# Performance work log

Hardware: AMD Instinct MI355X
Metric: run time of the kernel (lower is better)

Reference implementation:

```python
import jax, jax.numpy as jnp
from jax import lax
import numpy as np

C = 64      # channels
K = 3       # dynamic kernel size
N = 2       # batch
H = 256
W = 256
DOWN = 4    # avgpool factor


def _conv(x, w, b):
    # 'SAME' padding matches get_same_padding for odd kernels, dilation=1
    y = lax.conv_general_dilated(x, w, (1, 1), 'SAME',
                                 dimension_numbers=('NCHW', 'OIHW', 'NCHW'))
    return y + b[None, :, None, None]


def _resblock(x, w1, b1, w2, b2):
    out = jax.nn.leaky_relu(_conv(x, w1, b1), 0.1)
    return _conv(out, w2, b2) + x


def _block(x, ws1, bs1, ws2, bs2):
    # fixed small loop over 3 structurally distinct ResBlocks
    for i in range(ws1.shape[0]):
        x = _resblock(x, ws1[i], bs1[i], ws2[i], bs2[i])
    return x


def _avgpool(x, k):
    n, c, h, w = x.shape
    return x.reshape(n, c, h // k, k, w // k, k).mean(axis=(3, 5))


def _maxpool(x, k):
    n, c, h, w = x.shape
    return x.reshape(n, c, h // k, k, w // k, k).max(axis=(3, 5))


def _dyn_conv(x, wt, k):
    # per-pixel depthwise conv: out[n,c,h,w] = sum_{dh,dw} xpad[n,c,h+dh,w+dw] * wt[n, c*k*k + dh*k + dw, h, w]
    # (torch's unfold/permute flattening pairs feat tap (dh,dw) with kernel channel index dh*k+dw)
    n, c, h, w = x.shape
    pad = (k - 1) // 2
    xp = jnp.pad(x, ((0, 0), (0, 0), (pad, pad), (pad, pad)), mode='edge')  # replicate pad
    wr = wt.reshape(n, c, k * k, h, w)
    out = jnp.zeros_like(x)
    for dh in range(k):            # fixed 3x3 tap loop; avoids materializing the unfold tensor
        for dw in range(k):
            out = out + xp[:, :, dh:dh + h, dw:dw + w] * wr[:, :, dh * k + dw]
    return out


def setup_inputs() -> dict:
    key = jax.random.key(0)
    ks = jax.random.split(key, 11)
    s = 0.05  # small init so 6 residual blocks stay numerically tame
    return {
        'x': jax.random.normal(ks[0], (N, C, H, W), jnp.float32),
        'blk1_w1': jax.random.normal(ks[1], (3, C, C, K, K), jnp.float32) * s,
        'blk1_b1': jnp.zeros((3, C), jnp.float32),
        'blk1_w2': jax.random.normal(ks[2], (3, C, C, K, K), jnp.float32) * s,
        'blk1_b2': jnp.zeros((3, C), jnp.float32),
        'blk2_w1': jax.random.normal(ks[3], (3, C, C, K, K), jnp.float32) * s,
        'blk2_b1': jnp.zeros((3, C), jnp.float32),
        'blk2_w2': jax.random.normal(ks[4], (3, C, C, K, K), jnp.float32) * s,
        'blk2_b2': jnp.zeros((3, C), jnp.float32),
        'tok_w': jax.random.normal(ks[5], (K * K * C, C, 1, 1), jnp.float32) * s,
        'tok_b': jnp.zeros((K * K * C,), jnp.float32),
    }


def reference(x, blk1_w1, blk1_b1, blk1_w2, blk1_b2,
              blk2_w1, blk2_b1, blk2_w2, blk2_b2, tok_w, tok_b):
    y = _avgpool(x, DOWN)                                   # [N,C,H/4,W/4]
    y = _block(y, blk1_w1, blk1_b1, blk1_w2, blk1_b2)
    y = _maxpool(y, 2)                                      # [N,C,H/8,W/8]
    y = _block(y, blk2_w1, blk2_b1, blk2_w2, blk2_b2)
    wt = _conv(y, tok_w, tok_b)                             # [N,9C,H/8,W/8]
    n, ck2, hs, ws = wt.shape
    # F.interpolate(scale_factor=2*down, mode='bilinear', align_corners=False)
    wt = jax.image.resize(wt, (n, ck2, hs * 2 * DOWN, ws * 2 * DOWN), method='bilinear')
    return _dyn_conv(x, wt, K)
```

## Files before the change

### kernel.cpp

```cpp
#include <hip/hip_runtime.h>


__global__ __launch_bounds__(256) void avgpool4_k(const float* __restrict__ x,
                                                  float* __restrict__ y) {
    int idx = blockIdx.x * 256 + threadIdx.x;
    int wo = idx & 63;
    int ho = (idx >> 6) & 63;
    int cz = idx >> 12;
    const float* base = x + ((long)cz * 256 + ho * 4) * 256 + wo * 4;
    float s = 0.f;
#pragma unroll
    for (int r = 0; r < 4; ++r) {
        float4 v = *(const float4*)(base + r * 256);
        s += v.x + v.y + v.z + v.w;
    }
    y[idx] = s * 0.0625f;
}

template <int S, int CIB, int TW, int PXL>
__global__ __launch_bounds__(256) void conv3x3w_k(
    const float* __restrict__ in, const float* __restrict__ wgt,
    float* __restrict__ outp) {
    constexpr int KSN = 64 / CIB;
    constexpr int TH = 16;
    constexpr int NTW = S / TW, NTH = S / TH;
    constexpr int NT = NTW * NTH;
    constexpr int HW = TW + 2;
    constexpr int SROW = TW + 4;
    constexpr int TOT = CIB * 18 * HW;
    constexpr int NLD = (TOT + 255) / 256;
    constexpr int TAIL = TOT - (NLD - 1) * 256;
    __shared__ float s_in[CIB * 18 * SROW];
    __shared__ __align__(16) float s_w[CIB * 144];

    const int tid = threadIdx.x;
    int z = blockIdx.x;
    const int ks = z % KSN; z /= KSN;
    const int ocg = z & 3; z >>= 2;
    const int tile = z % NT;
    const int n = z / NT;
    const int th0 = (tile / NTW) * TH, tw0 = (tile % NTW) * TW;
    const int oc0 = ocg * 16;

    for (int i = tid; i < CIB * 144; i += 256) {
        int k = i / (CIB * 9);
        int rem = i - k * (CIB * 9);
        s_w[rem * 16 + k] = wgt[(oc0 + k) * 576 + ks * (CIB * 9) + rem];
    }

    const float* inb = in + ((long)n * 64 + ks * CIB) * (S * S);
#pragma unroll
    for (int j = 0; j < NLD; ++j) {
        int idx = tid + j * 256;
        bool slot = (j < NLD - 1) || (tid < TAIL);
        int t = slot ? idx : 0;
        int ci = t / (18 * HW);
        int rem = t - ci * (18 * HW);
        int r = rem / HW;
        int c = rem - r * HW;
        int gh = th0 + r - 1, gw = tw0 + c - 1;
        float v = 0.f;
        if (slot && (unsigned)gh < (unsigned)S && (unsigned)gw < (unsigned)S)
            v = inb[ci * (S * S) + gh * S + gw];
        if (slot) s_in[ci * (18 * SROW) + r * SROW + c] = v;
    }
    __syncthreads();

    const int lane = tid & 63;
    const int wid = tid >> 6;
    const int lx = lane & 3;
    const int ly = lane >> 2;
    const int px0 = lx * PXL;

    float acc[4][PXL];
#pragma unroll
    for (int k = 0; k < 4; ++k)
#pragma unroll
        for (int p = 0; p < PXL; ++p) acc[k][p] = 0.f;

#pragma unroll
    for (int ci = 0; ci < CIB; ++ci) {
        float xr[3][PXL + 2];
#pragma unroll
        for (int r = 0; r < 3; ++r) {
            const float* rp = &s_in[ci * (18 * SROW) + (ly + r) * SROW + px0];
#pragma unroll
            for (int q = 0; q < PXL / 4; ++q) {
                float4 a = *(const float4*)(rp + q * 4);
                xr[r][q * 4 + 0] = a.x; xr[r][q * 4 + 1] = a.y;
                xr[r][q * 4 + 2] = a.z; xr[r][q * 4 + 3] = a.w;
            }
            float2 b = *(const float2*)(rp + PXL);
            xr[r][PXL] = b.x; xr[r][PXL + 1] = b.y;
        }
#pragma unroll
        for (int dh = 0; dh < 3; ++dh)
#pragma unroll
            for (int dw = 0; dw < 3; ++dw) {
                float4 wv = *(const float4*)&s_w[(ci * 9 + dh * 3 + dw) * 16 + wid * 4];
#pragma unroll
                for (int p = 0; p < PXL; ++p) {
                    float xv = xr[dh][p + dw];
                    acc[0][p] += xv * wv.x;
                    acc[1][p] += xv * wv.y;
                    acc[2][p] += xv * wv.z;
                    acc[3][p] += xv * wv.w;
                }
            }
    }

    const int gy = th0 + ly, gx = tw0 + px0;
    const long pstride = (long)2 * 64 * S * S;
#pragma unroll
    for (int k = 0; k < 4; ++k) {
        long off = ks * pstride +
                   ((long)(n * 64 + oc0 + wid * 4 + k)) * (S * S) + gy * S + gx;
#pragma unroll
        for (int q = 0; q < PXL / 4; ++q) {
            float4 v;
            v.x = acc[k][q * 4 + 0]; v.y = acc[k][q * 4 + 1];
            v.z = acc[k][q * 4 + 2]; v.w = acc[k][q * 4 + 3];
            *(float4*)&outp[off + q * 4] = v;
        }
    }
}

template <int NP, int SSLOG, bool LRELU, bool RES>
__global__ __launch_bounds__(256) void comb_k(
    const float* __restrict__ P, const float* __restrict__ bias,
    const float* __restrict__ res, float* __restrict__ out) {
    const long pstride = (long)2 * 64 << SSLOG;
    long base = ((long)blockIdx.x * 256 + threadIdx.x) * 4;
    int c = (int)((base >> SSLOG) & 63);
    float4 v = *(const float4*)&P[base];
#pragma unroll
    for (int p = 1; p < NP; ++p) {
        float4 u = *(const float4*)&P[base + p * pstride];
        v.x += u.x; v.y += u.y; v.z += u.z; v.w += u.w;
    }
    float b = bias[c];
    v.x += b; v.y += b; v.z += b; v.w += b;
    if (LRELU) {
        v.x = v.x > 0.f ? v.x : 0.1f * v.x;
        v.y = v.y > 0.f ? v.y : 0.1f * v.y;
        v.z = v.z > 0.f ? v.z : 0.1f * v.z;
        v.w = v.w > 0.f ? v.w : 0.1f * v.w;
    }
    if (RES) {
        float4 r = *(const float4*)&res[base];
        v.x += r.x; v.y += r.y; v.z += r.z; v.w += r.w;
    }
    *(float4*)&out[base] = v;
}

template <int NP>
__global__ __launch_bounds__(256) void maxpool_comb_k(
    const float* __restrict__ Pb, const float* __restrict__ bias,
    const float* __restrict__ res, float* __restrict__ P) {
    int idx = blockIdx.x * 256 + threadIdx.x;
    int wo = idx & 31;
    int ho = (idx >> 5) & 31;
    int cz = idx >> 10;
    float bch = bias[cz & 63];
    float m = -3.4e38f;
#pragma unroll
    for (int dh = 0; dh < 2; ++dh)
#pragma unroll
        for (int dw = 0; dw < 2; ++dw) {
            long off = ((long)cz * 64 + ho * 2 + dh) * 64 + wo * 2 + dw;
            float y = bch + res[off];
#pragma unroll
            for (int p = 0; p < NP; ++p) y += Pb[off + (long)p * 524288];
            m = fmaxf(m, y);
        }
    P[idx] = m;
}

__global__ __launch_bounds__(256) void conv1x1_k(
    const float* __restrict__ in, const float* __restrict__ w,
    const float* __restrict__ b, float* __restrict__ out) {
    __shared__ float s_in[32 * 256];
    __shared__ __align__(16) float s_w[64 * 8];
    const int tid = threadIdx.x;
    const int p0 = blockIdx.x * 256;
    const int cog = blockIdx.y;
    const int n = blockIdx.z;

    for (int idx = tid; idx < 512; idx += 256) {
        int j = idx >> 6;
        int ci = idx & 63;
        s_w[ci * 8 + j] = w[(long)cog * 512 + idx];
    }

    float acc[8];
#pragma unroll
    for (int i = 0; i < 8; ++i) acc[i] = b[cog * 8 + i];

    float pf[32];
#pragma unroll
    for (int i = 0; i < 32; ++i)
        pf[i] = in[(long)(n * 64 + i) * 1024 + p0 + tid];

    for (int chunk = 0; chunk < 64; chunk += 32) {
        __syncthreads();
#pragma unroll
        for (int i = 0; i < 32; ++i) s_in[i * 256 + tid] = pf[i];
        __syncthreads();
        if (chunk + 32 < 64) {
#pragma unroll
            for (int i = 0; i < 32; ++i)
                pf[i] = in[(long)(n * 64 + chunk + 32 + i) * 1024 + p0 + tid];
        }
#pragma unroll 4
        for (int ci = 0; ci < 32; ++ci) {
            float v = s_in[ci * 256 + tid];
            float4 w0 = *(const float4*)&s_w[(chunk + ci) * 8];
            float4 w1 = *(const float4*)&s_w[(chunk + ci) * 8 + 4];
            acc[0] += v * w0.x; acc[1] += v * w0.y;
            acc[2] += v * w0.z; acc[3] += v * w0.w;
            acc[4] += v * w1.x; acc[5] += v * w1.y;
            acc[6] += v * w1.z; acc[7] += v * w1.w;
        }
    }
#pragma unroll
    for (int oc = 0; oc < 8; ++oc)
        out[(long)(n * 576 + cog * 8 + oc) * 1024 + p0 + tid] = acc[oc];
}

__global__ __launch_bounds__(256) void dynconv_k(
    const float* __restrict__ x, const float* __restrict__ wt,
    float* __restrict__ out) {
    __shared__ __align__(16) float s_x[10 * 132];
    __shared__ float s_wt[9 * 60];
    const int tid = threadIdx.x;
    const int tx = tid & 31;
    const int ty = tid >> 5;
    const int tw = (blockIdx.x & 1) * 128;
    const int th = (blockIdx.x >> 1) * 8;
    const int cz = blockIdx.y;

    const float* xb = x + (long)cz * 65536;
    for (int idx = tid; idx < 1300; idx += 256) {
        int r = idx / 130;
        int c = idx - r * 130;
        int gh = min(max(th + r - 1, 0), 255);
        int gw = min(max(tw + c - 1, 0), 255);
        s_x[r * 132 + c] = xb[gh * 256 + gw];
    }

    const int h0min = th / 8 - 1;
    const int w0min = tw / 8 - 1;
    const float* wtb = wt + (long)cz * 9 * 1024;
    for (int i = tid; i < 540; i += 256) {
        int tap = i / 60;
        int rem = i - tap * 60;
        int r = rem / 20;
        int c = rem - r * 20;
        if (c < 18) {
            int gr = min(max(h0min + r, 0), 31);
            int gc = min(max(w0min + c, 0), 31);
            s_wt[i] = wtb[tap * 1024 + gr * 32 + gc];
        }
    }

    const int h = th + ty;
    const int wbase = tw + tx * 4;
    float src_h = h * 0.125f - 0.4375f;
    int h0 = (int)floorf(src_h);
    float fh = src_h - (float)h0;
    int r0 = h0 - h0min;
    float src_w = wbase * 0.125f - 0.4375f;
    int w0 = (int)floorf(src_w);
    float fw0 = src_w - (float)w0;
    int j = w0 - w0min;

    __syncthreads();

    float vals[3][6];
#pragma unroll
    for (int r = 0; r < 3; ++r) {
        const float* rp = &s_x[(ty + r) * 132 + tx * 4];
        float4 a = *(const float4*)rp;
        float2 b = *(const float2*)(rp + 4);
        vals[r][0] = a.x; vals[r][1] = a.y; vals[r][2] = a.z;
        vals[r][3] = a.w; vals[r][4] = b.x; vals[r][5] = b.y;
    }

    float acc[4] = {0.f, 0.f, 0.f, 0.f};
#pragma unroll
    for (int dh = 0; dh < 3; ++dh)
#pragma unroll
        for (int dw = 0; dw < 3; ++dw) {
            const float* p = &s_wt[(dh * 3 + dw) * 60 + r0 * 20 + j];
            float t0 = p[0], t1 = p[1];
            float b0 = p[20], b1 = p[21];
            float c0 = t0 + fh * (b0 - t0);
            float c1 = t1 + fh * (b1 - t1);
            float d = c1 - c0;
#pragma unroll
            for (int jj = 0; jj < 4; ++jj) {
                float wv = c0 + (fw0 + 0.125f * jj) * d;
                acc[jj] += vals[dh][jj + dw] * wv;
            }
        }

    float4 o;
    o.x = acc[0]; o.y = acc[1]; o.z = acc[2]; o.w = acc[3];
    *(float4*)&out[(long)cz * 65536 + h * 256 + wbase] = o;
}

extern "C" void kernel_launch(void* const* d_in, const int* in_sizes, int n_in,
                              void* d_out, int out_size, void* d_ws, size_t ws_size,
                              hipStream_t stream) {
    const float* x    = (const float*)d_in[0];
    const float* b1w1 = (const float*)d_in[1];
    const float* b1b1 = (const float*)d_in[2];
    const float* b1w2 = (const float*)d_in[3];
    const float* b1b2 = (const float*)d_in[4];
    const float* b2w1 = (const float*)d_in[5];
    const float* b2b1 = (const float*)d_in[6];
    const float* b2w2 = (const float*)d_in[7];
    const float* b2b2 = (const float*)d_in[8];
    const float* tokw = (const float*)d_in[9];
    const float* tokb = (const float*)d_in[10];
    float* out = (float*)d_out;
    float* ws = (float*)d_ws;

    float* X0 = ws;
    float* X1 = ws + 524288;
    float* T  = ws + 1048576;
    float* P  = ws + 1572864;
    float* Pm = ws + 5767168;
    float* Q  = ws + 5898240;
    float* U  = ws + 6029312;
    float* WT = ws + 6160384;

    const int WSZ = 64 * 64 * 9;

    avgpool4_k<<<2048, 256, 0, stream>>>(x, X0);

    conv3x3w_k<64, 8, 32, 8><<<512, 256, 0, stream>>>(X0, b1w1 + 0 * WSZ, P);
    comb_k<8, 12, true,  false><<<512, 256, 0, stream>>>(P, b1b1 + 0, nullptr, T);
    conv3x3w_k<64, 8, 32, 8><<<512, 256, 0, stream>>>(T, b1w2 + 0 * WSZ, P);
    comb_k<8, 12, false, true ><<<512, 256, 0, stream>>>(P, b1b2 + 0, X0, X1);

    conv3x3w_k<64, 8, 32, 8><<<512, 256, 0, stream>>>(X1, b1w1 + 1 * WSZ, P);
    comb_k<8, 12, true,  false><<<512, 256, 0, stream>>>(P, b1b1 + 64, nullptr, T);
    conv3x3w_k<64, 8, 32, 8><<<512, 256, 0, stream>>>(T, b1w2 + 1 * WSZ, P);
    comb_k<8, 12, false, true ><<<512, 256, 0, stream>>>(P, b1b2 + 64, X1, X0);

    conv3x3w_k<64, 8, 32, 8><<<512, 256, 0, stream>>>(X0, b1w1 + 2 * WSZ, P);
    comb_k<8, 12, true,  false><<<512, 256, 0, stream>>>(P, b1b1 + 128, nullptr, T);
    conv3x3w_k<64, 8, 32, 8><<<512, 256, 0, stream>>>(T, b1w2 + 2 * WSZ, P);
    maxpool_comb_k<8><<<512, 256, 0, stream>>>(P, b1b2 + 128, X0, Pm);

    conv3x3w_k<32, 4, 16, 4><<<512, 256, 0, stream>>>(Pm, b2w1 + 0 * WSZ, P);
    comb_k<16, 10, true,  false><<<128, 256, 0, stream>>>(P, b2b1 + 0, nullptr, U);
    conv3x3w_k<32, 4, 16, 4><<<512, 256, 0, stream>>>(U, b2w2 + 0 * WSZ, P);
    comb_k<16, 10, false, true ><<<128, 256, 0, stream>>>(P, b2b2 + 0, Pm, Q);

    conv3x3w_k<32, 4, 16, 4><<<512, 256, 0, stream>>>(Q, b2w1 + 1 * WSZ, P);
    comb_k<16, 10, true,  false><<<128, 256, 0, stream>>>(P, b2b1 + 64, nullptr, U);
    conv3x3w_k<32, 4, 16, 4><<<512, 256, 0, stream>>>(U, b2w2 + 1 * WSZ, P);
    comb_k<16, 10, false, true ><<<128, 256, 0, stream>>>(P, b2b2 + 64, Q, Pm);

    conv3x3w_k<32, 4, 16, 4><<<512, 256, 0, stream>>>(Pm, b2w1 + 2 * WSZ, P);
    comb_k<16, 10, true,  false><<<128, 256, 0, stream>>>(P, b2b1 + 128, nullptr, U);
    conv3x3w_k<32, 4, 16, 4><<<512, 256, 0, stream>>>(U, b2w2 + 2 * WSZ, P);
    comb_k<16, 10, false, true ><<<128, 256, 0, stream>>>(P, b2b2 + 128, Pm, Q);

    conv1x1_k<<<dim3(4, 72, 2), 256, 0, stream>>>(Q, tokw, tokb, WT);

    dynconv_k<<<dim3(64, 128), 256, 0, stream>>>(x, WT, out);
}
```

Measured before the change: 371.7 us.

## Rewrite 3x3 conv with square tiles, wave-uniform scalar weight loads, fewer K splits

Replaces the shared-memory weight staging in the 3x3 conv with per-wave scalar loads straight from global memory, using readfirstlane so the compiler can treat the weight addresses as uniform. Tiles become 16x16 with 4 pixels per thread, and input-channel chunks double, which halves the number of K-split partial planes that the combine kernels must sum. The goal is less LDS traffic, less partial-sum memory traffic and fewer combine reads. The trade-off is smaller per-thread register blocking, so there is less reuse per loaded input value, and fewer blocks are launched in block 2.

```diff
diff --git a/kernel.cpp b/kernel.cpp
--- a/kernel.cpp
+++ b/kernel.cpp
@@ -17,21 +17,20 @@
     y[idx] = s * 0.0625f;
 }
 
-template <int S, int CIB, int TW, int PXL>
-__global__ __launch_bounds__(256) void conv3x3w_k(
+template <int S, int CIB>
+__global__ __launch_bounds__(256, 2) void conv3x3s_k(
     const float* __restrict__ in, const float* __restrict__ wgt,
     float* __restrict__ outp) {
     constexpr int KSN = 64 / CIB;
-    constexpr int TH = 16;
-    constexpr int NTW = S / TW, NTH = S / TH;
-    constexpr int NT = NTW * NTH;
-    constexpr int HW = TW + 2;
-    constexpr int SROW = TW + 4;
+    constexpr int T = 16;
+    constexpr int NT1 = S / T;
+    constexpr int NT = NT1 * NT1;
+    constexpr int HW = T + 2;
+    constexpr int SROW = 20;
     constexpr int TOT = CIB * 18 * HW;
     constexpr int NLD = (TOT + 255) / 256;
     constexpr int TAIL = TOT - (NLD - 1) * 256;
-    __shared__ float s_in[CIB * 18 * SROW];
-    __shared__ __align__(16) float s_w[CIB * 144];
+    __shared__ __align__(16) float s_in[CIB * 18 * SROW];
 
     const int tid = threadIdx.x;
     int z = blockIdx.x;
@@ -39,14 +38,8 @@
     const int ocg = z & 3; z >>= 2;
     const int tile = z % NT;
     const int n = z / NT;
-    const int th0 = (tile / NTW) * TH, tw0 = (tile % NTW) * TW;
+    const int th0 = (tile / NT1) * T, tw0 = (tile % NT1) * T;
     const int oc0 = ocg * 16;
-
-    for (int i = tid; i < CIB * 144; i += 256) {
-        int k = i / (CIB * 9);
-        int rem = i - k * (CIB * 9);
-        s_w[rem * 16 + k] = wgt[(oc0 + k) * 576 + ks * (CIB * 9) + rem];
-    }
 
     const float* inb = in + ((long)n * 64 + ks * CIB) * (S * S);
 #pragma unroll
@@ -67,61 +60,55 @@
     __syncthreads();
 
     const int lane = tid & 63;
-    const int wid = tid >> 6;
+    const int wid = __builtin_amdgcn_readfirstlane(tid >> 6);
     const int lx = lane & 3;
     const int ly = lane >> 2;
-    const int px0 = lx * PXL;
-
-    float acc[4][PXL];
+    const int px0 = lx * 4;
+
+    const float* wb = wgt + (long)(oc0 + wid * 4) * 576 + ks * (CIB * 9);
+
+    float acc[4][4];
 #pragma unroll
     for (int k = 0; k < 4; ++k)
 #pragma unroll
-        for (int p = 0; p < PXL; ++p) acc[k][p] = 0.f;
+        for (int p = 0; p < 4; ++p) acc[k][p] = 0.f;
 
 #pragma unroll
     for (int ci = 0; ci < CIB; ++ci) {
-        float xr[3][PXL + 2];
+        float xr[3][6];
 #pragma unroll
         for (int r = 0; r < 3; ++r) {
             const float* rp = &s_in[ci * (18 * SROW) + (ly + r) * SROW + px0];
-#pragma unroll
-            for (int q = 0; q < PXL / 4; ++q) {
-                float4 a = *(const float4*)(rp + q * 4);
-                xr[r][q * 4 + 0] = a.x; xr[r][q * 4 + 1] = a.y;
-                xr[r][q * 4 + 2] = a.z; xr[r][q * 4 + 3] = a.w;
+            float4 a = *(const float4*)rp;
+            float2 b = *(const float2*)(rp + 4);
+            xr[r][0] = a.x; xr[r][1] = a.y; xr[r][2] = a.z;
+            xr[r][3] = a.w; xr[r][4] = b.x; xr[r][5] = b.y;
+        }
+#pragma unroll
+        for (int k = 0; k < 4; ++k) {
+            const float* wk = wb + k * 576 + ci * 9;
+#pragma unroll
+            for (int dh = 0; dh < 3; ++dh) {
+                float w0 = wk[dh * 3 + 0];
+                float w1 = wk[dh * 3 + 1];
+                float w2 = wk[dh * 3 + 2];
+#pragma unroll
+                for (int p = 0; p < 4; ++p)
+                    acc[k][p] += xr[dh][p] * w0 + xr[dh][p + 1] * w1 +
+                                 xr[dh][p + 2] * w2;
             }
-            float2 b = *(const float2*)(rp + PXL);
-            xr[r][PXL] = b.x; xr[r][PXL + 1] = b.y;
-        }
-#pragma unroll
-        for (int dh = 0; dh < 3; ++dh)
-#pragma unroll
-            for (int dw = 0; dw < 3; ++dw) {
-                float4 wv = *(const float4*)&s_w[(ci * 9 + dh * 3 + dw) * 16 + wid * 4];
-#pragma unroll
-                for (int p = 0; p < PXL; ++p) {
-                    float xv = xr[dh][p + dw];
-                    acc[0][p] += xv * wv.x;
-                    acc[1][p] += xv * wv.y;
-                    acc[2][p] += xv * wv.z;
-                    acc[3][p] += xv * wv.w;
-                }
-            }
+        }
     }
 
     const int gy = th0 + ly, gx = tw0 + px0;
     const long pstride = (long)2 * 64 * S * S;
+    long off0 = ks * pstride +
+                ((long)(n * 64 + oc0 + wid * 4)) * (S * S) + gy * S + gx;
 #pragma unroll
     for (int k = 0; k < 4; ++k) {
-        long off = ks * pstride +
-                   ((long)(n * 64 + oc0 + wid * 4 + k)) * (S * S) + gy * S + gx;
-#pragma unroll
-        for (int q = 0; q < PXL / 4; ++q) {
-            float4 v;
-            v.x = acc[k][q * 4 + 0]; v.y = acc[k][q * 4 + 1];
-            v.z = acc[k][q * 4 + 2]; v.w = acc[k][q * 4 + 3];
-            *(float4*)&outp[off + q * 4] = v;
-        }
+        float4 v;
+        v.x = acc[k][0]; v.y = acc[k][1]; v.z = acc[k][2]; v.w = acc[k][3];
+        *(float4*)&outp[off0 + (long)k * (S * S)] = v;
     }
 }
 
@@ -339,35 +326,35 @@
 
     avgpool4_k<<<2048, 256, 0, stream>>>(x, X0);
 
-    conv3x3w_k<64, 8, 32, 8><<<512, 256, 0, stream>>>(X0, b1w1 + 0 * WSZ, P);
-    comb_k<8, 12, true,  false><<<512, 256, 0, stream>>>(P, b1b1 + 0, nullptr, T);
-    conv3x3w_k<64, 8, 32, 8><<<512, 256, 0, stream>>>(T, b1w2 + 0 * WSZ, P);
-    comb_k<8, 12, false, true ><<<512, 256, 0, stream>>>(P, b1b2 + 0, X0, X1);
-
-    conv3x3w_k<64, 8, 32, 8><<<512, 256, 0, stream>>>(X1, b1w1 + 1 * WSZ, P);
-    comb_k<8, 12, true,  false><<<512, 256, 0, stream>>>(P, b1b1 + 64, nullptr, T);
-    conv3x3w_k<64, 8, 32, 8><<<512, 256, 0, stream>>>(T, b1w2 + 1 * WSZ, P);
-    comb_k<8, 12, false, true ><<<512, 256, 0, stream>>>(P, b1b2 + 64, X1, X0);
-
-    conv3x3w_k<64, 8, 32, 8><<<512, 256, 0, stream>>>(X0, b1w1 + 2 * WSZ, P);
-    comb_k<8, 12, true,  false><<<512, 256, 0, stream>>>(P, b1b1 + 128, nullptr, T);
-    conv3x3w_k<64, 8, 32, 8><<<512, 256, 0, stream>>>(T, b1w2 + 2 * WSZ, P);
-    maxpool_comb_k<8><<<512, 256, 0, stream>>>(P, b1b2 + 128, X0, Pm);
-
-    conv3x3w_k<32, 4, 16, 4><<<512, 256, 0, stream>>>(Pm, b2w1 + 0 * WSZ, P);
-    comb_k<16, 10, true,  false><<<128, 256, 0, stream>>>(P, b2b1 + 0, nullptr, U);
-    conv3x3w_k<32, 4, 16, 4><<<512, 256, 0, stream>>>(U, b2w2 + 0 * WSZ, P);
-    comb_k<16, 10, false, true ><<<128, 256, 0, stream>>>(P, b2b2 + 0, Pm, Q);
-
-    conv3x3w_k<32, 4, 16, 4><<<512, 256, 0, stream>>>(Q, b2w1 + 1 * WSZ, P);
-    comb_k<16, 10, true,  false><<<128, 256, 0, stream>>>(P, b2b1 + 64, nullptr, U);
-    conv3x3w_k<32, 4, 16, 4><<<512, 256, 0, stream>>>(U, b2w2 + 1 * WSZ, P);
-    comb_k<16, 10, false, true ><<<128, 256, 0, stream>>>(P, b2b2 + 64, Q, Pm);
-
-    conv3x3w_k<32, 4, 16, 4><<<512, 256, 0, stream>>>(Pm, b2w1 + 2 * WSZ, P);
-    comb_k<16, 10, true,  false><<<128, 256, 0, stream>>>(P, b2b1 + 128, nullptr, U);
-    conv3x3w_k<32, 4, 16, 4><<<512, 256, 0, stream>>>(U, b2w2 + 2 * WSZ, P);
-    comb_k<16, 10, false, true ><<<128, 256, 0, stream>>>(P, b2b2 + 128, Pm, Q);
+    conv3x3s_k<64, 16><<<512, 256, 0, stream>>>(X0, b1w1 + 0 * WSZ, P);
+    comb_k<4, 12, true,  false><<<512, 256, 0, stream>>>(P, b1b1 + 0, nullptr, T);
+    conv3x3s_k<64, 16><<<512, 256, 0, stream>>>(T, b1w2 + 0 * WSZ, P);
+    comb_k<4, 12, false, true ><<<512, 256, 0, stream>>>(P, b1b2 + 0, X0, X1);
+
+    conv3x3s_k<64, 16><<<512, 256, 0, stream>>>(X1, b1w1 + 1 * WSZ, P);
+    comb_k<4, 12, true,  false><<<512, 256, 0, stream>>>(P, b1b1 + 64, nullptr, T);
+    conv3x3s_k<64, 16><<<512, 256, 0, stream>>>(T, b1w2 + 1 * WSZ, P);
+    comb_k<4, 12, false, true ><<<512, 256, 0, stream>>>(P, b1b2 + 64, X1, X0);
+
+    conv3x3s_k<64, 16><<<512, 256, 0, stream>>>(X0, b1w1 + 2 * WSZ, P);
+    comb_k<4, 12, true,  false><<<512, 256, 0, stream>>>(P, b1b1 + 128, nullptr, T);
+    conv3x3s_k<64, 16><<<512, 256, 0, stream>>>(T, b1w2 + 2 * WSZ, P);
+    maxpool_comb_k<4><<<512, 256, 0, stream>>>(P, b1b2 + 128, X0, Pm);
+
+    conv3x3s_k<32, 8><<<256, 256, 0, stream>>>(Pm, b2w1 + 0 * WSZ, P);
+    comb_k<8, 10, true,  false><<<128, 256, 0, stream>>>(P, b2b1 + 0, nullptr, U);
+    conv3x3s_k<32, 8><<<256, 256, 0, stream>>>(U, b2w2 + 0 * WSZ, P);
+    comb_k<8, 10, false, true ><<<128, 256, 0, stream>>>(P, b2b2 + 0, Pm, Q);
+
+    conv3x3s_k<32, 8><<<256, 256, 0, stream>>>(Q, b2w1 + 1 * WSZ, P);
+    comb_k<8, 10, true,  false><<<128, 256, 0, stream>>>(P, b2b1 + 64, nullptr, U);
+    conv3x3s_k<32, 8><<<256, 256, 0, stream>>>(U, b2w2 + 1 * WSZ, P);
+    comb_k<8, 10, false, true ><<<128, 256, 0, stream>>>(P, b2b2 + 64, Q, Pm);
+
+    conv3x3s_k<32, 8><<<256, 256, 0, stream>>>(Pm, b2w1 + 2 * WSZ, P);
+    comb_k<8, 10, true,  false><<<128, 256, 0, stream>>>(P, b2b1 + 128, nullptr, U);
+    conv3x3s_k<32, 8><<<256, 256, 0, stream>>>(U, b2w2 + 2 * WSZ, P);
+    comb_k<8, 10, false, true ><<<128, 256, 0, stream>>>(P, b2b2 + 128, Pm, Q);
 
     conv1x1_k<<<dim3(4, 72, 2), 256, 0, stream>>>(Q, tokw, tokb, WT);
 
```

After: 372.1 us. No clear change (+0.1%).
